# Performance work log

Hardware: AMD Instinct MI355X
Metric: run time of the kernel (lower is better)

Reference implementation:

```python
import jax, jax.numpy as jnp
import numpy as np

INV_SQRT2 = np.float32(2.0 ** -0.5)
EPS = 1e-5


def _bn5(x, g, b, m, v):
    # inference-mode BatchNorm3d over channel axis 1 of NCDHW
    r = (1, -1, 1, 1, 1)
    return (x - m.reshape(r)) * (g.reshape(r) * jax.lax.rsqrt(v.reshape(r) + EPS)) + b.reshape(r)


def _conv3d(x, w, b, dil=1, pad=0):
    out = jax.lax.conv_general_dilated(
        x, w, window_strides=(1, 1, 1), padding=[(pad, pad)] * 3,
        rhs_dilation=(dil, dil, dil),
        dimension_numbers=('NCDHW', 'OIDHW', 'NCDHW'))
    return out + b.reshape(1, -1, 1, 1, 1)


def _haar_dwt2(x):
    # pywt dwt2(x, 'haar', axes=(-3,-2)) for even-length axes.
    # axis -3 (D): a = approx, d = detail (pywt sign: (x0 - x1)/sqrt2)
    a = (x[:, :, 0::2] + x[:, :, 1::2]) * INV_SQRT2
    d = (x[:, :, 0::2] - x[:, :, 1::2]) * INV_SQRT2
    # axis -2 (H)
    LL = (a[:, :, :, 0::2] + a[:, :, :, 1::2]) * INV_SQRT2  # 'aa'
    HL = (a[:, :, :, 0::2] - a[:, :, :, 1::2]) * INV_SQRT2  # 'ad'
    LH = (d[:, :, :, 0::2] + d[:, :, :, 1::2]) * INV_SQRT2  # 'da'
    HH = (d[:, :, :, 0::2] - d[:, :, :, 1::2]) * INV_SQRT2  # 'dd'
    return LL, LH, HL, HH


def setup_inputs() -> dict:
    key = jax.random.key(0)
    ks = jax.random.split(key, 12)
    B, C1, D, H, W = 2, 60, 128, 128, 64
    CH, R = 64, 4  # gate channels, CH // reduction_ratio
    f32 = jnp.float32
    inp = {
        'x1': jax.random.normal(ks[0], (B, C1, D // 2, H // 2, W), f32),
        'x2': jax.random.normal(ks[1], (B, 1, D, H, W), f32),
        # BatchNorm3d(4) on dwt features
        'bn_g': jnp.ones(4, f32), 'bn_b': jnp.zeros(4, f32),
        'bn_m': jnp.zeros(4, f32), 'bn_v': jnp.ones(4, f32),
        # BAM channel gate: Linear(64->4), BN1d(4), Linear(4->64)
        'cg_w1': jax.random.normal(ks[2], (R, CH), f32) * 0.05,
        'cg_b1': jnp.zeros(R, f32),
        'cg_bng': jnp.ones(R, f32), 'cg_bnb': jnp.zeros(R, f32),
        'cg_bnm': jnp.zeros(R, f32), 'cg_bnv': jnp.ones(R, f32),
        'cg_w2': jax.random.normal(ks[3], (CH, R), f32) * 0.05,
        'cg_b2': jnp.zeros(CH, f32),
        # BAM spatial gate
        'sg_w0': jax.random.normal(ks[4], (R, CH, 1, 1, 1), f32) * 0.05,
        'sg_b0': jnp.zeros(R, f32),
        'sg_g0': jnp.ones(R, f32), 'sg_be0': jnp.zeros(R, f32),
        'sg_m0': jnp.zeros(R, f32), 'sg_v0': jnp.ones(R, f32),
        'sg_w1': jax.random.normal(ks[5], (R, R, 3, 3, 3), f32) * 0.05,
        'sg_b1': jnp.zeros(R, f32),
        'sg_g1': jnp.ones(R, f32), 'sg_be1': jnp.zeros(R, f32),
        'sg_m1': jnp.zeros(R, f32), 'sg_v1': jnp.ones(R, f32),
        'sg_w2': jax.random.normal(ks[6], (R, R, 3, 3, 3), f32) * 0.05,
        'sg_b2': jnp.zeros(R, f32),
        'sg_g2': jnp.ones(R, f32), 'sg_be2': jnp.zeros(R, f32),
        'sg_m2': jnp.zeros(R, f32), 'sg_v2': jnp.ones(R, f32),
        'sg_w3': jax.random.normal(ks[7], (1, R, 1, 1, 1), f32) * 0.05,
        'sg_b3': jnp.zeros(1, f32),
    }
    return inp


def reference(x1, x2, bn_g, bn_b, bn_m, bn_v,
              cg_w1, cg_b1, cg_bng, cg_bnb, cg_bnm, cg_bnv, cg_w2, cg_b2,
              sg_w0, sg_b0, sg_g0, sg_be0, sg_m0, sg_v0,
              sg_w1, sg_b1, sg_g1, sg_be1, sg_m1, sg_v1,
              sg_w2, sg_b2, sg_g2, sg_be2, sg_m2, sg_v2,
              sg_w3, sg_b3):
    LL, LH, HL, HH = _haar_dwt2(x2)
    dwt = jnp.concatenate([LL, LH, HL, HH], axis=1)          # [B,4,D/2,H/2,W]
    dwt = jax.nn.relu(_bn5(dwt, bn_g, bn_b, bn_m, bn_v))
    feat = jnp.concatenate([dwt, x1], axis=1)                # [B,64,D/2,H/2,W]

    # BAM channel gate
    pooled = feat.mean(axis=(2, 3, 4))                        # [B,64]
    h = pooled @ cg_w1.T + cg_b1
    h = jax.nn.relu((h - cg_bnm) * (cg_bng * jax.lax.rsqrt(cg_bnv + EPS)) + cg_bnb)
    att_c = (h @ cg_w2.T + cg_b2)[:, :, None, None, None]     # [B,64,1,1,1]

    # BAM spatial gate
    s = jax.nn.relu(_bn5(_conv3d(feat, sg_w0, sg_b0), sg_g0, sg_be0, sg_m0, sg_v0))
    s = jax.nn.relu(_bn5(_conv3d(s, sg_w1, sg_b1, dil=4, pad=4), sg_g1, sg_be1, sg_m1, sg_v1))
    s = jax.nn.relu(_bn5(_conv3d(s, sg_w2, sg_b2, dil=4, pad=4), sg_g2, sg_be2, sg_m2, sg_v2))
    att_s = _conv3d(s, sg_w3, sg_b3)                          # [B,1,D/2,H/2,W]

    scale = 1.0 + jax.nn.sigmoid(att_c + att_s)
    return (feat * scale, LL)
```

## Files before the change

kernel.cpp:

```cpp
#include <hip/hip_runtime.h>
#include <math.h>

#define EPSBN 1e-5f

typedef float f32x2 __attribute__((ext_vector_type(2)));
typedef float f32x4 __attribute__((ext_vector_type(4)));

constexpr int B   = 2;
constexpr int C1  = 60;
constexpr int NV  = 64 * 64 * 64;
constexpr int NBa = NV / 1024;
constexpr int NBc = NV / 512;

__global__ __launch_bounds__(256) void kA(
    const float* __restrict__ x1, const float* __restrict__ x2,
    const float* __restrict__ bn_g, const float* __restrict__ bn_b,
    const float* __restrict__ bn_m, const float* __restrict__ bn_v,
    const float* __restrict__ sg_w0, const float* __restrict__ sg_b0,
    const float* __restrict__ sg_g0, const float* __restrict__ sg_be0,
    const float* __restrict__ sg_m0, const float* __restrict__ sg_v0,
    float* __restrict__ dwtM, float* __restrict__ s0,
    float* __restrict__ part, float* __restrict__ outLL)
{
    __shared__ float wsumq[64][65];

    const int tid = threadIdx.x;
    const int qid = tid >> 2;

    float dsc[4], dsh[4], c0A[4], c0B[4];
    #pragma unroll
    for (int r = 0; r < 4; ++r) {
        float d = bn_g[r] * rsqrtf(bn_v[r] + EPSBN);
        dsc[r] = d; dsh[r] = bn_b[r] - bn_m[r] * d;
        float sc = sg_g0[r] * rsqrtf(sg_v0[r] + EPSBN);
        c0A[r] = sc; c0B[r] = (sg_b0[r] - sg_m0[r]) * sc + sg_be0[r];
    }

    const int b = blockIdx.y;
    const int v = blockIdx.x * 1024 + tid * 4;
    const int x = v & 63, y = (v >> 6) & 63, z = v >> 12;

    const float* px2 = x2 + (size_t)b * (128 * 128 * 64);
    const size_t i00 = ((size_t)(2 * z) * 128 + 2 * y) * 64 + x;
    const float4 p00 = *(const float4*)(px2 + i00);
    const float4 p01 = *(const float4*)(px2 + i00 + 64);
    const float4 p10 = *(const float4*)(px2 + i00 + 8192);
    const float4 p11 = *(const float4*)(px2 + i00 + 8256);
    const float* q00 = (const float*)&p00; const float* q01 = (const float*)&p01;
    const float* q10 = (const float*)&p10; const float* q11 = (const float*)&p11;

    float tv[4][4], llv[4];
    #pragma unroll
    for (int vi = 0; vi < 4; ++vi) {
        float a = q00[vi], bb = q01[vi], c = q10[vi], d = q11[vi];
        float LL = 0.5f * (a + bb + c + d);
        float LH = 0.5f * (a + bb - c - d);
        float HL = 0.5f * (a - bb + c - d);
        float HH = 0.5f * (a - bb - c + d);
        llv[vi] = LL;
        tv[vi][0] = fmaxf(LL * dsc[0] + dsh[0], 0.f);
        tv[vi][1] = fmaxf(LH * dsc[1] + dsh[1], 0.f);
        tv[vi][2] = fmaxf(HL * dsc[2] + dsh[2], 0.f);
        tv[vi][3] = fmaxf(HH * dsc[3] + dsh[3], 0.f);
    }
    {
        f32x4 ll4 = { llv[0], llv[1], llv[2], llv[3] };
        __builtin_nontemporal_store(ll4, (f32x4*)(outLL + (size_t)b * NV + v));
    }

    float acc[4][4] = {};
    #pragma unroll
    for (int c = 0; c < 4; ++c) {
        #pragma unroll
        for (int vi = 0; vi < 4; ++vi) {
            float t = tv[vi][c];
            #pragma unroll
            for (int r = 0; r < 4; ++r) acc[vi][r] += sg_w0[r * 64 + c] * t;
        }
        float rs = tv[0][c] + tv[1][c] + tv[2][c] + tv[3][c];
        rs += __shfl_xor(rs, 1);
        rs += __shfl_xor(rs, 2);
        if ((tid & 3) == 0) wsumq[c][qid] = rs;
        *(float4*)(dwtM + ((size_t)b * 4 + c) * NV + v) =
            make_float4(tv[0][c], tv[1][c], tv[2][c], tv[3][c]);
    }

    const float* px1 = x1 + (size_t)b * C1 * NV + v;
    #pragma unroll 2
    for (int c = 0; c < C1; ++c) {
        const float4 f = *(const float4*)(px1 + (size_t)c * NV);
        const float* fv = (const float*)&f;
        #pragma unroll
        for (int r = 0; r < 4; ++r) {
            const float w = sg_w0[r * 64 + 4 + c];
            #pragma unroll
            for (int vi = 0; vi < 4; ++vi) acc[vi][r] += w * fv[vi];
        }
        float rs = f.x + f.y + f.z + f.w;
        rs += __shfl_xor(rs, 1);
        rs += __shfl_xor(rs, 2);
        if ((tid & 3) == 0) wsumq[4 + c][qid] = rs;
    }

    float4* ps0 = (float4*)s0 + (size_t)b * NV + v;
    #pragma unroll
    for (int vi = 0; vi < 4; ++vi)
        ps0[vi] = make_float4(fmaxf(acc[vi][0] * c0A[0] + c0B[0], 0.f),
                              fmaxf(acc[vi][1] * c0A[1] + c0B[1], 0.f),
                              fmaxf(acc[vi][2] * c0A[2] + c0B[2], 0.f),
                              fmaxf(acc[vi][3] * c0A[3] + c0B[3], 0.f));

    __syncthreads();
    if (tid < 64) {
        const float* rowp = &wsumq[tid][0];
        float p = 0.f;
        #pragma unroll
        for (int i = 0; i < 64; ++i) p += rowp[i];
        part[((size_t)b * 64 + tid) * NBa + blockIdx.x] = p;
    }
}

__global__ __launch_bounds__(256) void kConv1(
    const float* __restrict__ sin_,
    const float* __restrict__ w, const float* __restrict__ bias,
    const float* __restrict__ g, const float* __restrict__ be,
    const float* __restrict__ m, const float* __restrict__ vv,
    const float* __restrict__ part,
    const float* __restrict__ cg_w1, const float* __restrict__ cg_b1,
    const float* __restrict__ cg_bng, const float* __restrict__ cg_bnb,
    const float* __restrict__ cg_bnm, const float* __restrict__ cg_bnv,
    const float* __restrict__ cg_w2, const float* __restrict__ cg_b2,
    float* __restrict__ ec,
    float* __restrict__ outp)
{
    const int tid = threadIdx.x;
    const int b = blockIdx.y;

    if (blockIdx.x == NBc) {
        __shared__ float pooled[64];
        __shared__ float h[4];
        const int c = tid >> 2, q = tid & 3;
        const float4* pp = (const float4*)(part + ((size_t)b * 64 + c) * NBa + q * 64);
        float sm = 0.f;
        #pragma unroll
        for (int i = 0; i < 16; ++i) { float4 f = pp[i]; sm += f.x + f.y + f.z + f.w; }
        sm += __shfl_xor(sm, 1);
        sm += __shfl_xor(sm, 2);
        if (q == 0) pooled[c] = sm * (1.0f / NV);
        __syncthreads();
        if (tid < 4) {
            float a = cg_b1[tid];
            for (int cc = 0; cc < 64; ++cc) a += pooled[cc] * cg_w1[tid * 64 + cc];
            float sc = cg_bng[tid] * rsqrtf(cg_bnv[tid] + EPSBN);
            h[tid] = fmaxf((a - cg_bnm[tid]) * sc + cg_bnb[tid], 0.f);
        }
        __syncthreads();
        if (tid < 64) {
            float a = cg_b2[tid];
            #pragma unroll
            for (int r = 0; r < 4; ++r) a += h[r] * cg_w2[tid * 4 + r];
            ec[b * 64 + tid] = __expf(-a);
        }
        return;
    }

    __shared__ float4 wl4[108];
    if (tid < 108) {
        const int t = tid >> 2, r = tid & 3;
        wl4[tid] = make_float4(w[r * 108 +      t], w[r * 108 +  27 + t],
                               w[r * 108 + 54 + t], w[r * 108 +  81 + t]);
    }
    float cAr[4], cBr[4];
    #pragma unroll
    for (int r = 0; r < 4; ++r) {
        float sc = g[r] * rsqrtf(vv[r] + EPSBN);
        cAr[r] = sc;
        cBr[r] = (bias[r] - m[r]) * sc + be[r];
    }
    __syncthreads();

    const int v = blockIdx.x * 512 + tid * 2;
    const int x = v & 63, y = (v >> 6) & 63, z = v >> 12;
    const float4* pin = (const float4*)sin_ + (size_t)b * NV;

    float acc[2][4] = {};
    #pragma unroll
    for (int kz = -1; kz <= 1; ++kz) {
        const int zz = z + 4 * kz;
        if ((unsigned)zz >= 64u) continue;
        #pragma unroll
        for (int ky = -1; ky <= 1; ++ky) {
            const int yy = y + 4 * ky;
            if ((unsigned)yy >= 64u) continue;
            #pragma unroll
            for (int kx = -1; kx <= 1; ++kx) {
                const int xx = x + 4 * kx;
                if ((unsigned)xx >= 64u) continue;
                const int t = (kz + 1) * 9 + (ky + 1) * 3 + (kx + 1);
                const int vt = zz * 4096 + yy * 64 + xx;
                const float4 w0 = wl4[t * 4 + 0];
                const float4 w1 = wl4[t * 4 + 1];
                const float4 w2 = wl4[t * 4 + 2];
                const float4 w3 = wl4[t * 4 + 3];
                #pragma unroll
                for (int vi = 0; vi < 2; ++vi) {
                    const float4 tap = pin[vt + vi];
                    acc[vi][0] += w0.x * tap.x + w0.y * tap.y + w0.z * tap.z + w0.w * tap.w;
                    acc[vi][1] += w1.x * tap.x + w1.y * tap.y + w1.z * tap.z + w1.w * tap.w;
                    acc[vi][2] += w2.x * tap.x + w2.y * tap.y + w2.z * tap.z + w2.w * tap.w;
                    acc[vi][3] += w3.x * tap.x + w3.y * tap.y + w3.z * tap.z + w3.w * tap.w;
                }
            }
        }
    }

    float4* po = (float4*)outp + (size_t)b * NV + v;
    #pragma unroll
    for (int vi = 0; vi < 2; ++vi)
        po[vi] = make_float4(fmaxf(acc[vi][0] * cAr[0] + cBr[0], 0.f),
                             fmaxf(acc[vi][1] * cAr[1] + cBr[1], 0.f),
                             fmaxf(acc[vi][2] * cAr[2] + cBr[2], 0.f),
                             fmaxf(acc[vi][3] * cAr[3] + cBr[3], 0.f));
}

__global__ __launch_bounds__(256) void kMulF(
    const float* __restrict__ x1,
    const float* __restrict__ dwtM,
    const float* __restrict__ s1,
    const float* __restrict__ w, const float* __restrict__ bias,
    const float* __restrict__ g, const float* __restrict__ be,
    const float* __restrict__ m, const float* __restrict__ vv,
    const float* __restrict__ w3, const float* __restrict__ b3,
    const float* __restrict__ ec,
    float* __restrict__ out0)
{
    const int tid = threadIdx.x;
    const int b = blockIdx.x >> 9;
    const int vb = (blockIdx.x & 511) * 512;

    __shared__ float4 wl4[108];
    __shared__ float ecs[64];
    __shared__ float esb[512];
    if (tid < 108) {
        const int t = tid >> 2, r = tid & 3;
        wl4[tid] = make_float4(w[r * 108 +      t], w[r * 108 +  27 + t],
                               w[r * 108 + 54 + t], w[r * 108 +  81 + t]);
    }
    if (tid < 64) ecs[tid] = ec[b * 64 + tid];
    float cAr[4], cBr[4], w3l[4];
    #pragma unroll
    for (int r = 0; r < 4; ++r) {
        float sc = g[r] * rsqrtf(vv[r] + EPSBN);
        cAr[r] = sc;
        cBr[r] = (bias[r] - m[r]) * sc + be[r];
        w3l[r] = w3[r];
    }
    const float b3l = b3[0];
    __syncthreads();

    {
        const int v = vb + tid * 2;
        const int x = v & 63, y = (v >> 6) & 63, z = v >> 12;
        const float4* pin = (const float4*)s1 + (size_t)b * NV;
        float acc[2][4] = {};
        #pragma unroll
        for (int kz = -1; kz <= 1; ++kz) {
            const int zz = z + 4 * kz;
            if ((unsigned)zz >= 64u) continue;
            #pragma unroll
            for (int ky = -1; ky <= 1; ++ky) {
                const int yy = y + 4 * ky;
                if ((unsigned)yy >= 64u) continue;
                #pragma unroll
                for (int kx = -1; kx <= 1; ++kx) {
                    const int xx = x + 4 * kx;
                    if ((unsigned)xx >= 64u) continue;
                    const int t = (kz + 1) * 9 + (ky + 1) * 3 + (kx + 1);
                    const int vt = zz * 4096 + yy * 64 + xx;
                    const float4 w0 = wl4[t * 4 + 0];
                    const float4 w1 = wl4[t * 4 + 1];
                    const float4 w2 = wl4[t * 4 + 2];
                    const float4 w3q = wl4[t * 4 + 3];
                    #pragma unroll
                    for (int vi = 0; vi < 2; ++vi) {
                        const float4 tap = pin[vt + vi];
                        acc[vi][0] += w0.x * tap.x + w0.y * tap.y + w0.z * tap.z + w0.w * tap.w;
                        acc[vi][1] += w1.x * tap.x + w1.y * tap.y + w1.z * tap.z + w1.w * tap.w;
                        acc[vi][2] += w2.x * tap.x + w2.y * tap.y + w2.z * tap.z + w2.w * tap.w;
                        acc[vi][3] += w3q.x * tap.x + w3q.y * tap.y + w3q.z * tap.z + w3q.w * tap.w;
                    }
                }
            }
        }
        #pragma unroll
        for (int vi = 0; vi < 2; ++vi) {
            float r0 = fmaxf(acc[vi][0] * cAr[0] + cBr[0], 0.f);
            float r1 = fmaxf(acc[vi][1] * cAr[1] + cBr[1], 0.f);
            float r2 = fmaxf(acc[vi][2] * cAr[2] + cBr[2], 0.f);
            float r3 = fmaxf(acc[vi][3] * cAr[3] + cBr[3], 0.f);
            esb[tid * 2 + vi] =
                __expf(-(b3l + w3l[0] * r0 + w3l[1] * r1 + w3l[2] * r2 + w3l[3] * r3));
        }
    }
    __syncthreads();

    const int q = tid & 127;
    const int v = vb + q * 4;
    const int ch0 = (tid >> 7) * 32;
    const float es0 = esb[q * 4 + 0], es1 = esb[q * 4 + 1];
    const float es2 = esb[q * 4 + 2], es3 = esb[q * 4 + 3];

    float* po = out0 + ((size_t)b * 64 + ch0) * NV + v;
    #pragma unroll 4
    for (int cc = 0; cc < 32; ++cc) {
        const int c = ch0 + cc;
        const float* basep = (c < 4)
            ? dwtM + ((size_t)b * 4 + c) * NV
            : x1   + ((size_t)b * C1 + (c - 4)) * NV;
        const float4 in4 = *(const float4*)(basep + v);
        const float e = ecs[c];
        f32x4 o;
        o.x = in4.x * (1.f + __builtin_amdgcn_rcpf(1.f + e * es0));
        o.y = in4.y * (1.f + __builtin_amdgcn_rcpf(1.f + e * es1));
        o.z = in4.z * (1.f + __builtin_amdgcn_rcpf(1.f + e * es2));
        o.w = in4.w * (1.f + __builtin_amdgcn_rcpf(1.f + e * es3));
        __builtin_nontemporal_store(o, (f32x4*)(po + (size_t)cc * NV));
    }
}

extern "C" void kernel_launch(void* const* d_in, const int* in_sizes, int n_in,
                              void* d_out, int out_size, void* d_ws, size_t ws_size,
                              hipStream_t stream)
{
    const float* x1 = (const float*)d_in[0];
    const float* x2 = (const float*)d_in[1];
    const float* bn_g = (const float*)d_in[2];
    const float* bn_b = (const float*)d_in[3];
    const float* bn_m = (const float*)d_in[4];
    const float* bn_v = (const float*)d_in[5];
    const float* cg_w1 = (const float*)d_in[6];
    const float* cg_b1 = (const float*)d_in[7];
    const float* cg_bng = (const float*)d_in[8];
    const float* cg_bnb = (const float*)d_in[9];
    const float* cg_bnm = (const float*)d_in[10];
    const float* cg_bnv = (const float*)d_in[11];
    const float* cg_w2 = (const float*)d_in[12];
    const float* cg_b2 = (const float*)d_in[13];
    const float* sg_w0 = (const float*)d_in[14];
    const float* sg_b0 = (const float*)d_in[15];
    const float* sg_g0 = (const float*)d_in[16];
    const float* sg_be0 = (const float*)d_in[17];
    const float* sg_m0 = (const float*)d_in[18];
    const float* sg_v0 = (const float*)d_in[19];
    const float* sg_w1 = (const float*)d_in[20];
    const float* sg_b1 = (const float*)d_in[21];
    const float* sg_g1 = (const float*)d_in[22];
    const float* sg_be1 = (const float*)d_in[23];
    const float* sg_m1 = (const float*)d_in[24];
    const float* sg_v1 = (const float*)d_in[25];
    const float* sg_w2 = (const float*)d_in[26];
    const float* sg_b2 = (const float*)d_in[27];
    const float* sg_g2 = (const float*)d_in[28];
    const float* sg_be2 = (const float*)d_in[29];
    const float* sg_m2 = (const float*)d_in[30];
    const float* sg_v2 = (const float*)d_in[31];
    const float* sg_w3 = (const float*)d_in[32];
    const float* sg_b3 = (const float*)d_in[33];

    float* ws = (float*)d_ws;
    float* dwtM = ws;
    float* s0   = ws + 2097152;
    float* s1   = ws + 4194304;
    float* part = ws + 6291456;
    float* ec   = ws + 6324224;

    float* out0  = (float*)d_out;
    float* outLL = out0 + (size_t)B * 64 * NV;

    dim3 blk(256);
    kA<<<dim3(NBa, B), blk, 0, stream>>>(x1, x2, bn_g, bn_b, bn_m, bn_v,
                                         sg_w0, sg_b0, sg_g0, sg_be0, sg_m0, sg_v0,
                                         dwtM, s0, part, outLL);
    kConv1<<<dim3(NBc + 1, B), blk, 0, stream>>>(s0, sg_w1, sg_b1, sg_g1, sg_be1, sg_m1, sg_v1,
                                                 part, cg_w1, cg_b1, cg_bng, cg_bnb, cg_bnm, cg_bnv,
                                                 cg_w2, cg_b2, ec, s1);
    kMulF<<<dim3(1024), blk, 0, stream>>>(x1, dwtM, s1, sg_w2, sg_b2, sg_g2, sg_be2, sg_m2, sg_v2,
                                          sg_w3, sg_b3, ec, out0);
}
```

Measured before the change: 100.3 us.

## Recompute DWT features in final kernel instead of materialising dwt buffer

kA stops writing the 4-channel DWT buffer and the LL output. kMulF now re-reads x2, recomputes the Haar transform plus BN/ReLU into shared memory, writes LL, and uses those values directly for the first four output channels. This removes a 4-channel intermediate write and re-read through global memory in exchange for a second read of x2 (4 values per voxel) and extra shared memory in kMulF. The channel loop is also split into two specialised branches, and unroll factors are raised.

```diff
diff --git a/kernel.cpp b/kernel.cpp
--- a/kernel.cpp
+++ b/kernel.cpp
@@ -19,8 +19,8 @@
     const float* __restrict__ sg_w0, const float* __restrict__ sg_b0,
     const float* __restrict__ sg_g0, const float* __restrict__ sg_be0,
     const float* __restrict__ sg_m0, const float* __restrict__ sg_v0,
-    float* __restrict__ dwtM, float* __restrict__ s0,
-    float* __restrict__ part, float* __restrict__ outLL)
+    float* __restrict__ s0,
+    float* __restrict__ part)
 {
     __shared__ float wsumq[64][65];
 
@@ -49,7 +49,7 @@
     const float* q00 = (const float*)&p00; const float* q01 = (const float*)&p01;
     const float* q10 = (const float*)&p10; const float* q11 = (const float*)&p11;
 
-    float tv[4][4], llv[4];
+    float tv[4][4];
     #pragma unroll
     for (int vi = 0; vi < 4; ++vi) {
         float a = q00[vi], bb = q01[vi], c = q10[vi], d = q11[vi];
@@ -57,16 +57,11 @@
         float LH = 0.5f * (a + bb - c - d);
         float HL = 0.5f * (a - bb + c - d);
         float HH = 0.5f * (a - bb - c + d);
-        llv[vi] = LL;
         tv[vi][0] = fmaxf(LL * dsc[0] + dsh[0], 0.f);
         tv[vi][1] = fmaxf(LH * dsc[1] + dsh[1], 0.f);
         tv[vi][2] = fmaxf(HL * dsc[2] + dsh[2], 0.f);
         tv[vi][3] = fmaxf(HH * dsc[3] + dsh[3], 0.f);
     }
-    {
-        f32x4 ll4 = { llv[0], llv[1], llv[2], llv[3] };
-        __builtin_nontemporal_store(ll4, (f32x4*)(outLL + (size_t)b * NV + v));
-    }
 
     float acc[4][4] = {};
     #pragma unroll
@@ -81,12 +76,10 @@
         rs += __shfl_xor(rs, 1);
         rs += __shfl_xor(rs, 2);
         if ((tid & 3) == 0) wsumq[c][qid] = rs;
-        *(float4*)(dwtM + ((size_t)b * 4 + c) * NV + v) =
-            make_float4(tv[0][c], tv[1][c], tv[2][c], tv[3][c]);
     }
 
     const float* px1 = x1 + (size_t)b * C1 * NV + v;
-    #pragma unroll 2
+    #pragma unroll 4
     for (int c = 0; c < C1; ++c) {
         const float4 f = *(const float4*)(px1 + (size_t)c * NV);
         const float* fv = (const float*)&f;
@@ -225,14 +218,17 @@
 
 __global__ __launch_bounds__(256) void kMulF(
     const float* __restrict__ x1,
-    const float* __restrict__ dwtM,
+    const float* __restrict__ x2,
+    const float* __restrict__ bn_g, const float* __restrict__ bn_b,
+    const float* __restrict__ bn_m, const float* __restrict__ bn_v,
     const float* __restrict__ s1,
     const float* __restrict__ w, const float* __restrict__ bias,
     const float* __restrict__ g, const float* __restrict__ be,
     const float* __restrict__ m, const float* __restrict__ vv,
     const float* __restrict__ w3, const float* __restrict__ b3,
     const float* __restrict__ ec,
-    float* __restrict__ out0)
+    float* __restrict__ out0,
+    float* __restrict__ outLL)
 {
     const int tid = threadIdx.x;
     const int b = blockIdx.x >> 9;
@@ -241,19 +237,22 @@
     __shared__ float4 wl4[108];
     __shared__ float ecs[64];
     __shared__ float esb[512];
+    __shared__ float dwtb[512][4];
     if (tid < 108) {
         const int t = tid >> 2, r = tid & 3;
         wl4[tid] = make_float4(w[r * 108 +      t], w[r * 108 +  27 + t],
                                w[r * 108 + 54 + t], w[r * 108 +  81 + t]);
     }
     if (tid < 64) ecs[tid] = ec[b * 64 + tid];
-    float cAr[4], cBr[4], w3l[4];
+    float cAr[4], cBr[4], w3l[4], dsc[4], dsh[4];
     #pragma unroll
     for (int r = 0; r < 4; ++r) {
         float sc = g[r] * rsqrtf(vv[r] + EPSBN);
         cAr[r] = sc;
         cBr[r] = (bias[r] - m[r]) * sc + be[r];
         w3l[r] = w3[r];
+        float d = bn_g[r] * rsqrtf(bn_v[r] + EPSBN);
+        dsc[r] = d; dsh[r] = bn_b[r] - bn_m[r] * d;
     }
     const float b3l = b3[0];
     __syncthreads();
@@ -261,6 +260,35 @@
     {
         const int v = vb + tid * 2;
         const int x = v & 63, y = (v >> 6) & 63, z = v >> 12;
+
+        const float* px2 = x2 + (size_t)b * (128 * 128 * 64);
+        const size_t i00 = ((size_t)(2 * z) * 128 + 2 * y) * 64 + x;
+        const float2 p00 = *(const float2*)(px2 + i00);
+        const float2 p01 = *(const float2*)(px2 + i00 + 64);
+        const float2 p10 = *(const float2*)(px2 + i00 + 8192);
+        const float2 p11 = *(const float2*)(px2 + i00 + 8256);
+        const float* q00 = (const float*)&p00; const float* q01 = (const float*)&p01;
+        const float* q10 = (const float*)&p10; const float* q11 = (const float*)&p11;
+        float llv[2];
+        #pragma unroll
+        for (int vi = 0; vi < 2; ++vi) {
+            float a = q00[vi], bb = q01[vi], c = q10[vi], d = q11[vi];
+            float LL = 0.5f * (a + bb + c + d);
+            float LH = 0.5f * (a + bb - c - d);
+            float HL = 0.5f * (a - bb + c - d);
+            float HH = 0.5f * (a - bb - c + d);
+            llv[vi] = LL;
+            float4 tv = make_float4(fmaxf(LL * dsc[0] + dsh[0], 0.f),
+                                    fmaxf(LH * dsc[1] + dsh[1], 0.f),
+                                    fmaxf(HL * dsc[2] + dsh[2], 0.f),
+                                    fmaxf(HH * dsc[3] + dsh[3], 0.f));
+            *(float4*)&dwtb[tid * 2 + vi][0] = tv;
+        }
+        {
+            f32x2 ll2 = { llv[0], llv[1] };
+            __builtin_nontemporal_store(ll2, (f32x2*)(outLL + (size_t)b * NV + v));
+        }
+
         const float4* pin = (const float4*)s1 + (size_t)b * NV;
         float acc[2][4] = {};
         #pragma unroll
@@ -311,20 +339,51 @@
     const float es2 = esb[q * 4 + 2], es3 = esb[q * 4 + 3];
 
     float* po = out0 + ((size_t)b * 64 + ch0) * NV + v;
-    #pragma unroll 4
-    for (int cc = 0; cc < 32; ++cc) {
-        const int c = ch0 + cc;
-        const float* basep = (c < 4)
-            ? dwtM + ((size_t)b * 4 + c) * NV
-            : x1   + ((size_t)b * C1 + (c - 4)) * NV;
-        const float4 in4 = *(const float4*)(basep + v);
-        const float e = ecs[c];
-        f32x4 o;
-        o.x = in4.x * (1.f + __builtin_amdgcn_rcpf(1.f + e * es0));
-        o.y = in4.y * (1.f + __builtin_amdgcn_rcpf(1.f + e * es1));
-        o.z = in4.z * (1.f + __builtin_amdgcn_rcpf(1.f + e * es2));
-        o.w = in4.w * (1.f + __builtin_amdgcn_rcpf(1.f + e * es3));
-        __builtin_nontemporal_store(o, (f32x4*)(po + (size_t)cc * NV));
+
+    if (ch0 == 0) {
+        float4 dq0 = *(const float4*)&dwtb[q * 4 + 0][0];
+        float4 dq1 = *(const float4*)&dwtb[q * 4 + 1][0];
+        float4 dq2 = *(const float4*)&dwtb[q * 4 + 2][0];
+        float4 dq3 = *(const float4*)&dwtb[q * 4 + 3][0];
+        const float dv0[4] = { dq0.x, dq0.y, dq0.z, dq0.w };
+        const float dv1[4] = { dq1.x, dq1.y, dq1.z, dq1.w };
+        const float dv2[4] = { dq2.x, dq2.y, dq2.z, dq2.w };
+        const float dv3[4] = { dq3.x, dq3.y, dq3.z, dq3.w };
+        #pragma unroll
+        for (int cc = 0; cc < 4; ++cc) {
+            const float e = ecs[cc];
+            f32x4 o;
+            o.x = dv0[cc] * (1.f + __builtin_amdgcn_rcpf(1.f + e * es0));
+            o.y = dv1[cc] * (1.f + __builtin_amdgcn_rcpf(1.f + e * es1));
+            o.z = dv2[cc] * (1.f + __builtin_amdgcn_rcpf(1.f + e * es2));
+            o.w = dv3[cc] * (1.f + __builtin_amdgcn_rcpf(1.f + e * es3));
+            __builtin_nontemporal_store(o, (f32x4*)(po + (size_t)cc * NV));
+        }
+        const float* px = x1 + (size_t)b * C1 * NV + v;
+        #pragma unroll 7
+        for (int cc = 4; cc < 32; ++cc) {
+            const float4 in4 = *(const float4*)(px + (size_t)(cc - 4) * NV);
+            const float e = ecs[cc];
+            f32x4 o;
+            o.x = in4.x * (1.f + __builtin_amdgcn_rcpf(1.f + e * es0));
+            o.y = in4.y * (1.f + __builtin_amdgcn_rcpf(1.f + e * es1));
+            o.z = in4.z * (1.f + __builtin_amdgcn_rcpf(1.f + e * es2));
+            o.w = in4.w * (1.f + __builtin_amdgcn_rcpf(1.f + e * es3));
+            __builtin_nontemporal_store(o, (f32x4*)(po + (size_t)cc * NV));
+        }
+    } else {
+        const float* px = x1 + ((size_t)b * C1 + 28) * NV + v;
+        #pragma unroll 8
+        for (int cc = 0; cc < 32; ++cc) {
+            const float4 in4 = *(const float4*)(px + (size_t)cc * NV);
+            const float e = ecs[32 + cc];
+            f32x4 o;
+            o.x = in4.x * (1.f + __builtin_amdgcn_rcpf(1.f + e * es0));
+            o.y = in4.y * (1.f + __builtin_amdgcn_rcpf(1.f + e * es1));
+            o.z = in4.z * (1.f + __builtin_amdgcn_rcpf(1.f + e * es2));
+            o.w = in4.w * (1.f + __builtin_amdgcn_rcpf(1.f + e * es3));
+            __builtin_nontemporal_store(o, (f32x4*)(po + (size_t)cc * NV));
+        }
     }
 }
 
@@ -368,11 +427,10 @@
     const float* sg_b3 = (const float*)d_in[33];
 
     float* ws = (float*)d_ws;
-    float* dwtM = ws;
-    float* s0   = ws + 2097152;
-    float* s1   = ws + 4194304;
-    float* part = ws + 6291456;
-    float* ec   = ws + 6324224;
+    float* s0   = ws;
+    float* s1   = ws + 2097152;
+    float* part = ws + 4194304;
+    float* ec   = ws + 4227072;
 
     float* out0  = (float*)d_out;
     float* outLL = out0 + (size_t)B * 64 * NV;
@@ -380,10 +438,11 @@
     dim3 blk(256);
     kA<<<dim3(NBa, B), blk, 0, stream>>>(x1, x2, bn_g, bn_b, bn_m, bn_v,
                                          sg_w0, sg_b0, sg_g0, sg_be0, sg_m0, sg_v0,
-                                         dwtM, s0, part, outLL);
+                                         s0, part);
     kConv1<<<dim3(NBc + 1, B), blk, 0, stream>>>(s0, sg_w1, sg_b1, sg_g1, sg_be1, sg_m1, sg_v1,
                                                  part, cg_w1, cg_b1, cg_bng, cg_bnb, cg_bnm, cg_bnv,
                                                  cg_w2, cg_b2, ec, s1);
-    kMulF<<<dim3(1024), blk, 0, stream>>>(x1, dwtM, s1, sg_w2, sg_b2, sg_g2, sg_be2, sg_m2, sg_v2,
-                                          sg_w3, sg_b3, ec, out0);
+    kMulF<<<dim3(1024), blk, 0, stream>>>(x1, x2, bn_g, bn_b, bn_m, bn_v,
+                                          s1, sg_w2, sg_b2, sg_g2, sg_be2, sg_m2, sg_v2,
+                                          sg_w3, sg_b3, ec, out0, outLL);
 }
```

After: 99.12 us (median of 2 runs). About the same (-1.2%).
